# Kernel optimization log

Hardware: AMD Instinct MI355X
Metric: run time of the kernel (lower is better)

Reference implementation:

```python
import jax, jax.numpy as jnp
import numpy as np

EMBED = 256
HEADS = 8
HEAD_DIM = EMBED // HEADS
POOL = 2
H_FEAT = 64
W_FEAT = 64
SCALE = HEAD_DIM ** -0.5
POOL_COMP = float(np.log(POOL * POOL))  # log(pool_size^2) logit compensation


def setup_inputs() -> dict:
    key = jax.random.key(0)
    ks = jax.random.split(key, 11)
    B, Nq = 1, H_FEAT * W_FEAT          # 4096 query tokens (one frame)
    num_spatial = 4 * H_FEAT * W_FEAT   # 4 memory frames -> 16384 spatial tokens
    n_ptr = 64                          # object pointer tokens (not pooled)
    s = 1.0 / np.sqrt(EMBED)
    inp = {
        "q": jax.random.normal(ks[0], (B, Nq, EMBED), jnp.float32),
        "k": jax.random.normal(ks[1], (B, num_spatial + n_ptr, EMBED), jnp.float32),
        "v": jax.random.normal(ks[2], (B, num_spatial + n_ptr, EMBED), jnp.float32),
        "Wq": jax.random.normal(ks[3], (EMBED, EMBED), jnp.float32) * s,
        "bq": jax.random.normal(ks[4], (EMBED,), jnp.float32) * 0.01,
        "Wk": jax.random.normal(ks[5], (EMBED, EMBED), jnp.float32) * s,
        "bk": jax.random.normal(ks[6], (EMBED,), jnp.float32) * 0.01,
        "Wv": jax.random.normal(ks[7], (EMBED, EMBED), jnp.float32) * s,
        "bv": jax.random.normal(ks[8], (EMBED,), jnp.float32) * 0.01,
        "Wo": jax.random.normal(ks[9], (EMBED, EMBED), jnp.float32) * s,
        "bo": jax.random.normal(ks[10], (EMBED,), jnp.float32) * 0.01,
        "num_spatial_mem": num_spatial,
    }
    return inp


def _pool_spatial(tokens, num_spatial):
    """Avg-pool spatial tokens with POOLxPOOL windows; keep pointer tokens."""
    B, N, C = tokens.shape
    sp = tokens[:, :num_spatial, :]
    ptr = tokens[:, num_spatial:, :]
    frames = num_spatial // (H_FEAT * W_FEAT)
    hp, wp = H_FEAT // POOL, W_FEAT // POOL
    sp = sp.reshape(B, frames, hp, POOL, wp, POOL, C).mean(axis=(3, 5))
    sp = sp.reshape(B, frames * hp * wp, C)
    return jnp.concatenate([sp, ptr], axis=1), frames * hp * wp


def _heads(x):
    B, N, _ = x.shape
    return x.reshape(B, N, HEADS, HEAD_DIM).transpose(0, 2, 1, 3)  # (B,h,N,d)


def reference(q, k, v, Wq, bq, Wk, bk, Wv, bv, Wo, bo, num_spatial_mem):
    B, Nq, _ = q.shape
    qp = q @ Wq + bq
    k_pooled, n_sp_pooled = _pool_spatial(k, num_spatial_mem)
    v_pooled, _ = _pool_spatial(v, num_spatial_mem)
    kp = k_pooled @ Wk + bk
    vp = v_pooled @ Wv + bv
    qh, kh, vh = _heads(qp), _heads(kp), _heads(vp)
    logits = jnp.einsum('bhqd,bhkd->bhqk', qh, kh) * SCALE
    # additive bias on the pooled-key subset only
    logits = logits.at[..., :n_sp_pooled].add(POOL_COMP)
    attn = jax.nn.softmax(logits, axis=-1)
    out = jnp.einsum('bhqk,bhkd->bhqd', attn, vh)
    out = out.transpose(0, 2, 1, 3).reshape(B, Nq, EMBED)
    return out @ Wo + bo
```

## Files before the change

kernel.cpp:

```cpp
#include <hip/hip_runtime.h>
#include <hip/hip_bf16.h>
#include <cstdint>

#define NQ 4096
#define NK 4160
#define NSP 16384
#define E 256
#define HD 32
#define SC2E 0.2550348652937f
#define C2_SP  -12.426950408889634f
#define C2_PTR -14.426950408889634f

typedef __attribute__((ext_vector_type(4))) float f32x4;
typedef __attribute__((ext_vector_type(8))) __bf16 bf16x8;
typedef __attribute__((ext_vector_type(4))) __bf16 bf16x4;

__global__ __launch_bounds__(256) void prep_kernel(
    const float* __restrict__ q, const float* __restrict__ k, const float* __restrict__ v,
    const float* __restrict__ Wq, const float* __restrict__ Wk,
    const float* __restrict__ Wv, const float* __restrict__ Wo,
    __bf16* __restrict__ qhi, __bf16* __restrict__ khi, __bf16* __restrict__ vhi,
    __bf16* __restrict__ wthi, __bf16* __restrict__ wtlo)
{
  __shared__ float tl[32][33];
  const int b = blockIdx.x, t = threadIdx.x;
  if (b < 1024) {
    const float4 f = *(const float4*)(q + (size_t)b * 1024 + t * 4);
    bf16x4 o;
    o[0] = (__bf16)f.x; o[1] = (__bf16)f.y; o[2] = (__bf16)f.z; o[3] = (__bf16)f.w;
    *(bf16x4*)(qhi + (size_t)b * 1024 + t * 4) = o;
  } else if (b < 5184) {
    const int p = b - 1024;
    float kv, vv;
    if (p < 4096) {
      int f = p >> 10, hp = (p >> 5) & 31, wp = p & 31;
      size_t r0 = (size_t)(f * 4096 + hp * 128 + wp * 2) * E + t;
      kv = 0.25f * (k[r0] + k[r0 + E] + k[r0 + 64 * E] + k[r0 + 65 * E]);
      vv = 0.25f * (v[r0] + v[r0 + E] + v[r0 + 64 * E] + v[r0 + 65 * E]);
    } else {
      size_t r = (size_t)(NSP + (p - 4096)) * E + t;
      kv = k[r]; vv = v[r];
    }
    khi[(size_t)p * E + t] = (__bf16)kv;
    vhi[(size_t)p * E + t] = (__bf16)vv;
  } else {
    const int wb = b - 5184;
    const int wsel = wb >> 6, tile = wb & 63;
    const float* W = (wsel == 0) ? Wq : (wsel == 1) ? Wk : (wsel == 2) ? Wv : Wo;
    __bf16* oh = wthi + (size_t)wsel * 65536;
    __bf16* ol = wtlo + (size_t)wsel * 65536;
    const int tr = (tile >> 3) * 32, tc = (tile & 7) * 32;
    const int rr = t >> 3, cc = (t & 7) * 4;
    *(float4*)&tl[rr][cc] = *(const float4*)(W + (size_t)(tr + rr) * E + tc + cc);
    __syncthreads();
    bf16x4 hv, lv;
#pragma unroll
    for (int i = 0; i < 4; ++i) {
      float x = tl[cc + i][rr];
      __bf16 bh = (__bf16)x;
      hv[i] = bh;
      lv[i] = (__bf16)(x - (float)bh);
    }
    *(bf16x4*)(oh + (size_t)(tc + rr) * E + tr + cc) = hv;
    *(bf16x4*)(ol + (size_t)(tc + rr) * E + tr + cc) = lv;
  }
}

template<int MODE>
__device__ __forceinline__ void gemm_body(
    const __bf16* __restrict__ X, const __bf16* __restrict__ XL,
    const __bf16* __restrict__ WTH, const __bf16* __restrict__ WTL,
    const float* __restrict__ bias, void* __restrict__ Y, int r0)
{
  const int t = threadIdx.x;
  const int lane = t & 63, ql = lane & 15, g = lane >> 4;
  const int w = t >> 6, c0 = w * 64;

  const __bf16* xp  = X + (size_t)(r0 + ql) * E + g * 8;
  const __bf16* xlp = (MODE == 3) ? XL + (size_t)(r0 + ql) * E + g * 8 : nullptr;
  const __bf16* wh0 = WTH + (size_t)(c0 + ql) * E + g * 8;
  const __bf16* wl0 = (MODE == 3) ? WTL + (size_t)(c0 + ql) * E + g * 8 : nullptr;

  f32x4 acc[4] = {};
#pragma unroll
  for (int k0 = 0; k0 < 8; ++k0) {
    bf16x8 a = *(const bf16x8*)(xp + k0 * 32);
    bf16x8 al{};
    if (MODE == 3) al = *(const bf16x8*)(xlp + k0 * 32);
#pragma unroll
    for (int j = 0; j < 4; ++j) {
      bf16x8 bh = *(const bf16x8*)(wh0 + (size_t)j * 16 * E + k0 * 32);
      if (MODE == 2) {
        acc[j] = __builtin_amdgcn_mfma_f32_16x16x32_bf16(bh, a, acc[j], 0, 0, 0);
      } else {
        acc[j] = __builtin_amdgcn_mfma_f32_16x16x32_bf16(a, bh, acc[j], 0, 0, 0);
        if (MODE == 3) {
          bf16x8 bl = *(const bf16x8*)(wl0 + (size_t)j * 16 * E + k0 * 32);
          acc[j] = __builtin_amdgcn_mfma_f32_16x16x32_bf16(al, bh, acc[j], 0, 0, 0);
          acc[j] = __builtin_amdgcn_mfma_f32_16x16x32_bf16(a, bl, acc[j], 0, 0, 0);
        }
      }
    }
  }

  if (MODE == 0 || MODE == 1) {
    const int NN = (MODE == 0) ? NQ : NK;
#pragma unroll
    for (int j = 0; j < 4; ++j) {
      const int c = c0 + 16 * j + ql;
      const float bv = bias[c];
      const int hh = c >> 5, d = c & 31;
      __bf16* dst = (__bf16*)Y + (size_t)hh * NN * HD + d;
#pragma unroll
      for (int r = 0; r < 4; ++r) {
        const int n = r0 + g * 4 + r;
        float o = acc[j][r] + bv;
        if (MODE == 0) o *= SC2E;
        dst[(size_t)n * HD] = (__bf16)o;
      }
    }
  } else if (MODE == 2) {
    const int n = r0 + ql;
    const int wi = n & 31;
    const int pos = ((wi & 15) >> 2) * 8 + (wi & 3) + 4 * ((wi >> 4) & 1);
    const size_t nb = (size_t)(n >> 5) * 32 + pos;
#pragma unroll
    for (int j = 0; j < 4; ++j)
#pragma unroll
      for (int r = 0; r < 4; ++r) {
        const int ch = c0 + 16 * j + g * 4 + r;
        const int hh = ch >> 5, d = ch & 31;
        ((__bf16*)Y)[(size_t)(hh * HD + d) * NK + nb] = (__bf16)(acc[j][r] + bias[ch]);
      }
  } else {
#pragma unroll
    for (int j = 0; j < 4; ++j) {
      const int c = c0 + 16 * j + ql;
      const float bv = bias[c];
#pragma unroll
      for (int r = 0; r < 4; ++r) {
        const int n = r0 + g * 4 + r;
        ((float*)Y)[(size_t)n * E + c] = acc[j][r] + bv;
      }
    }
  }
}

__global__ __launch_bounds__(256) void gemm_qkv(
    const __bf16* __restrict__ qhi, const __bf16* __restrict__ khi, const __bf16* __restrict__ vhi,
    const __bf16* __restrict__ wthi, const __bf16* __restrict__ wtlo,
    const float* __restrict__ bq, const float* __restrict__ bk, const float* __restrict__ bv,
    __bf16* __restrict__ qb, __bf16* __restrict__ kb, __bf16* __restrict__ vtp)
{
  const int b = blockIdx.x;
  if (b < 256) {
    gemm_body<0>(qhi, nullptr, wthi, nullptr, bq, qb, b * 16);
  } else if (b < 516) {
    gemm_body<1>(khi, nullptr, wthi + 65536, nullptr, bk, kb, (b - 256) * 16);
  } else {
    gemm_body<2>(vhi, nullptr, wthi + 2 * 65536, nullptr, bv, vtp, (b - 516) * 16);
  }
}

__global__ __launch_bounds__(256) void gemm_o(
    const __bf16* __restrict__ ahi, const __bf16* __restrict__ alo,
    const __bf16* __restrict__ wthi, const __bf16* __restrict__ wtlo,
    const float* __restrict__ bo, float* __restrict__ out)
{
  gemm_body<3>(ahi, alo, wthi, wtlo, bo, out, blockIdx.x * 16);
}

__global__ __launch_bounds__(512, 4) void attn_kernel(
    const __bf16* __restrict__ qb, const __bf16* __restrict__ kb,
    const __bf16* __restrict__ vtp, __bf16* __restrict__ ahi, __bf16* __restrict__ alo)
{
  __shared__ float OUT[4][64][36];
  __shared__ float LS[4][64];

  const int t = threadIdx.x;
  const int w = t >> 6, lane = t & 63;
  const int ql = lane & 15, g = lane >> 4;
  const int b = blockIdx.x;
  const int h = b & 7, qt = b >> 3;
  const int n0 = qt * 64;

  bf16x8 bq[4];
#pragma unroll
  for (int f = 0; f < 4; ++f)
    bq[f] = *(const bf16x8*)(qb + ((size_t)h * NQ + n0 + f * 16 + ql) * HD + g * 8);

  const int st = w * 16 + (w < 2 ? w : 2);
  const int nt = 16 + (w < 2 ? 1 : 0);

  const __bf16* kp = kb  + ((size_t)h * NK + st * 32 + ql) * HD + g * 8;
  const __bf16* vp = vtp + ((size_t)(h * HD) + ql) * NK + st * 32 + g * 8;
  const __bf16* vq = vp + (size_t)16 * NK;

  f32x4 o0[4] = {}, o1[4] = {};
  float ls[4] = {0.f, 0.f, 0.f, 0.f};

  bf16x8 kf0 = *(const bf16x8*)(kp);
  bf16x8 kf1 = *(const bf16x8*)(kp + 512);
  bf16x8 vf0 = *(const bf16x8*)(vp);
  bf16x8 vf1 = *(const bf16x8*)(vq);

#define TILE(C2V)                                                                   \
  _Pragma("unroll")                                                                 \
  for (int f = 0; f < 4; ++f) {                                                     \
    f32x4 s0 = __builtin_amdgcn_mfma_f32_16x16x32_bf16(kf0, bq[f], C2V, 0, 0, 0);   \
    f32x4 s1 = __builtin_amdgcn_mfma_f32_16x16x32_bf16(kf1, bq[f], C2V, 0, 0, 0);   \
    float e0 = exp2f(s0[0]), e1 = exp2f(s0[1]), e2 = exp2f(s0[2]), e3 = exp2f(s0[3]);\
    float e4 = exp2f(s1[0]), e5 = exp2f(s1[1]), e6 = exp2f(s1[2]), e7 = exp2f(s1[3]);\
    ls[f] += ((e0 + e1) + (e2 + e3)) + ((e4 + e5) + (e6 + e7));                     \
    bf16x8 p;                                                                       \
    p[0] = (__bf16)e0; p[1] = (__bf16)e1; p[2] = (__bf16)e2; p[3] = (__bf16)e3;     \
    p[4] = (__bf16)e4; p[5] = (__bf16)e5; p[6] = (__bf16)e6; p[7] = (__bf16)e7;     \
    o0[f] = __builtin_amdgcn_mfma_f32_16x16x32_bf16(p, vf0, o0[f], 0, 0, 0);        \
    o1[f] = __builtin_amdgcn_mfma_f32_16x16x32_bf16(p, vf1, o1[f], 0, 0, 0);        \
  }

  for (int it = 0; it < nt - 1; ++it) {
    bf16x8 nk0 = *(const bf16x8*)(kp + (size_t)(it + 1) * 1024);
    bf16x8 nk1 = *(const bf16x8*)(kp + (size_t)(it + 1) * 1024 + 512);
    bf16x8 nv0 = *(const bf16x8*)(vp + (size_t)(it + 1) * 32);
    bf16x8 nv1 = *(const bf16x8*)(vq + (size_t)(it + 1) * 32);
    const float c2 = (st + it < 128) ? C2_SP : C2_PTR;
    const f32x4 c2v = {c2, c2, c2, c2};
    TILE(c2v)
    kf0 = nk0; kf1 = nk1; vf0 = nv0; vf1 = nv1;
  }
  {
    const float c2 = (st + nt - 1 < 128) ? C2_SP : C2_PTR;
    const f32x4 c2v = {c2, c2, c2, c2};
    TILE(c2v)
  }
#undef TILE

#pragma unroll
  for (int f = 0; f < 4; ++f) {
    ls[f] += __shfl_xor(ls[f], 16);
    ls[f] += __shfl_xor(ls[f], 32);
  }

  if (w < 4) {
#pragma unroll
    for (int f = 0; f < 4; ++f) {
#pragma unroll
      for (int r = 0; r < 4; ++r) {
        OUT[w][f * 16 + g * 4 + r][ql]      = o0[f][r];
        OUT[w][f * 16 + g * 4 + r][16 + ql] = o1[f][r];
      }
      if (g == 0) LS[w][f * 16 + ql] = ls[f];
    }
  }
  __syncthreads();
  if (w >= 4) {
    const int w4 = w - 4;
#pragma unroll
    for (int f = 0; f < 4; ++f) {
#pragma unroll
      for (int r = 0; r < 4; ++r) {
        OUT[w4][f * 16 + g * 4 + r][ql]      += o0[f][r];
        OUT[w4][f * 16 + g * 4 + r][16 + ql] += o1[f][r];
      }
      if (g == 0) LS[w4][f * 16 + ql] += ls[f];
    }
  }
  __syncthreads();

  {
    const int q = t >> 3, d0 = (t & 7) * 4;
    f32x4 s = *(const f32x4*)&OUT[0][q][d0];
    float lsum = LS[0][q];
#pragma unroll
    for (int w2 = 1; w2 < 4; ++w2) {
      s += *(const f32x4*)&OUT[w2][q][d0];
      lsum += LS[w2][q];
    }
    const float inv = 1.0f / lsum;
    bf16x4 hv, lv;
#pragma unroll
    for (int i = 0; i < 4; ++i) {
      float o = s[i] * inv;
      __bf16 bh = (__bf16)o;
      hv[i] = bh;
      lv[i] = (__bf16)(o - (float)bh);
    }
    const size_t off = (size_t)(n0 + q) * E + h * HD + d0;
    *(bf16x4*)(ahi + off) = hv;
    *(bf16x4*)(alo + off) = lv;
  }
}

extern "C" void kernel_launch(void* const* d_in, const int* in_sizes, int n_in,
                              void* d_out, int out_size, void* d_ws, size_t ws_size,
                              hipStream_t stream)
{
  const float* q  = (const float*)d_in[0];
  const float* k  = (const float*)d_in[1];
  const float* v  = (const float*)d_in[2];
  const float* Wq = (const float*)d_in[3];
  const float* bq = (const float*)d_in[4];
  const float* Wk = (const float*)d_in[5];
  const float* bk = (const float*)d_in[6];
  const float* Wv = (const float*)d_in[7];
  const float* bv = (const float*)d_in[8];
  const float* Wo = (const float*)d_in[9];
  const float* bo = (const float*)d_in[10];
  float* out = (float*)d_out;

  char* wsp = (char*)d_ws;
  __bf16* qhi  = (__bf16*)(wsp);
  __bf16* khi  = (__bf16*)(wsp + 2097152);
  __bf16* vhi  = (__bf16*)(wsp + 4227072);
  __bf16* wthi = (__bf16*)(wsp + 6356992);
  __bf16* wtlo = (__bf16*)(wsp + 6881280);
  __bf16* qbb  = (__bf16*)(wsp + 7405568);
  __bf16* kbb  = (__bf16*)(wsp + 9502720);
  __bf16* vtp  = (__bf16*)(wsp + 11632640);
  __bf16* ahi  = (__bf16*)(wsp + 13762560);
  __bf16* alo  = (__bf16*)(wsp + 15859712);

  prep_kernel<<<5440, 256, 0, stream>>>(q, k, v, Wq, Wk, Wv, Wo, qhi, khi, vhi, wthi, wtlo);
  gemm_qkv<<<776, 256, 0, stream>>>(qhi, khi, vhi, wthi, wtlo, bq, bk, bv, qbb, kbb, vtp);
  attn_kernel<<<512, 512, 0, stream>>>(qbb, kbb, vtp, ahi, alo);
  gemm_o<<<256, 256, 0, stream>>>(ahi, alo, wthi + 3 * 65536, wtlo + 3 * 65536, bo, out);
}
```

Baseline: 86.01 us.

## Fuse input pooling and bf16 conversion into QKV projection GEMM

After: 69.98 us. -18.6%, faster.

```diff
diff --git a/kernel.cpp b/kernel.cpp
--- a/kernel.cpp
+++ b/kernel.cpp
@@ -15,91 +15,91 @@
 typedef __attribute__((ext_vector_type(8))) __bf16 bf16x8;
 typedef __attribute__((ext_vector_type(4))) __bf16 bf16x4;
 
-__global__ __launch_bounds__(256) void prep_kernel(
-    const float* __restrict__ q, const float* __restrict__ k, const float* __restrict__ v,
+__global__ __launch_bounds__(256) void wprep_kernel(
     const float* __restrict__ Wq, const float* __restrict__ Wk,
     const float* __restrict__ Wv, const float* __restrict__ Wo,
-    __bf16* __restrict__ qhi, __bf16* __restrict__ khi, __bf16* __restrict__ vhi,
     __bf16* __restrict__ wthi, __bf16* __restrict__ wtlo)
 {
   __shared__ float tl[32][33];
   const int b = blockIdx.x, t = threadIdx.x;
-  if (b < 1024) {
-    const float4 f = *(const float4*)(q + (size_t)b * 1024 + t * 4);
-    bf16x4 o;
-    o[0] = (__bf16)f.x; o[1] = (__bf16)f.y; o[2] = (__bf16)f.z; o[3] = (__bf16)f.w;
-    *(bf16x4*)(qhi + (size_t)b * 1024 + t * 4) = o;
-  } else if (b < 5184) {
-    const int p = b - 1024;
-    float kv, vv;
-    if (p < 4096) {
-      int f = p >> 10, hp = (p >> 5) & 31, wp = p & 31;
-      size_t r0 = (size_t)(f * 4096 + hp * 128 + wp * 2) * E + t;
-      kv = 0.25f * (k[r0] + k[r0 + E] + k[r0 + 64 * E] + k[r0 + 65 * E]);
-      vv = 0.25f * (v[r0] + v[r0 + E] + v[r0 + 64 * E] + v[r0 + 65 * E]);
+  const int wsel = b >> 6, tile = b & 63;
+  const float* W = (wsel == 0) ? Wq : (wsel == 1) ? Wk : (wsel == 2) ? Wv : Wo;
+  __bf16* oh = wthi + (size_t)wsel * 65536;
+  __bf16* ol = wtlo + (size_t)wsel * 65536;
+  const int tr = (tile >> 3) * 32, tc = (tile & 7) * 32;
+  const int rr = t >> 3, cc = (t & 7) * 4;
+  *(float4*)&tl[rr][cc] = *(const float4*)(W + (size_t)(tr + rr) * E + tc + cc);
+  __syncthreads();
+  bf16x4 hv, lv;
+#pragma unroll
+  for (int i = 0; i < 4; ++i) {
+    float x = tl[cc + i][rr];
+    __bf16 bh = (__bf16)x;
+    hv[i] = bh;
+    lv[i] = (__bf16)(x - (float)bh);
+  }
+  *(bf16x4*)(oh + (size_t)(tc + rr) * E + tr + cc) = hv;
+  *(bf16x4*)(ol + (size_t)(tc + rr) * E + tr + cc) = lv;
+}
+
+template<int MODE>
+__device__ __forceinline__ void qkv_body(
+    const float* __restrict__ Xsrc, const __bf16* __restrict__ WTH,
+    const float* __restrict__ bias, void* __restrict__ Y, int r0)
+{
+  __shared__ __bf16 Xs[16][264];
+  const int t = threadIdx.x;
+
+  {
+    const int pr = t >> 4, f4 = t & 15;
+    const int p = r0 + pr;
+    float4 x[4];
+    if (MODE == 0) {
+      const float* src = Xsrc + (size_t)p * E + f4 * 4;
+#pragma unroll
+      for (int j = 0; j < 4; ++j) x[j] = *(const float4*)(src + j * 64);
+    } else if (p < 4096) {
+      const int fr = p >> 10, hp = (p >> 5) & 31, wp = p & 31;
+      const float* src = Xsrc + (size_t)(fr * 4096 + hp * 128 + wp * 2) * E + f4 * 4;
+#pragma unroll
+      for (int j = 0; j < 4; ++j) {
+        float4 a = *(const float4*)(src + j * 64);
+        float4 b = *(const float4*)(src + j * 64 + E);
+        float4 c = *(const float4*)(src + j * 64 + 64 * E);
+        float4 d = *(const float4*)(src + j * 64 + 65 * E);
+        x[j].x = 0.25f * (a.x + b.x + c.x + d.x);
+        x[j].y = 0.25f * (a.y + b.y + c.y + d.y);
+        x[j].z = 0.25f * (a.z + b.z + c.z + d.z);
+        x[j].w = 0.25f * (a.w + b.w + c.w + d.w);
+      }
     } else {
-      size_t r = (size_t)(NSP + (p - 4096)) * E + t;
-      kv = k[r]; vv = v[r];
-    }
-    khi[(size_t)p * E + t] = (__bf16)kv;
-    vhi[(size_t)p * E + t] = (__bf16)vv;
-  } else {
-    const int wb = b - 5184;
-    const int wsel = wb >> 6, tile = wb & 63;
-    const float* W = (wsel == 0) ? Wq : (wsel == 1) ? Wk : (wsel == 2) ? Wv : Wo;
-    __bf16* oh = wthi + (size_t)wsel * 65536;
-    __bf16* ol = wtlo + (size_t)wsel * 65536;
-    const int tr = (tile >> 3) * 32, tc = (tile & 7) * 32;
-    const int rr = t >> 3, cc = (t & 7) * 4;
-    *(float4*)&tl[rr][cc] = *(const float4*)(W + (size_t)(tr + rr) * E + tc + cc);
-    __syncthreads();
-    bf16x4 hv, lv;
-#pragma unroll
-    for (int i = 0; i < 4; ++i) {
-      float x = tl[cc + i][rr];
-      __bf16 bh = (__bf16)x;
-      hv[i] = bh;
-      lv[i] = (__bf16)(x - (float)bh);
-    }
-    *(bf16x4*)(oh + (size_t)(tc + rr) * E + tr + cc) = hv;
-    *(bf16x4*)(ol + (size_t)(tc + rr) * E + tr + cc) = lv;
-  }
-}
-
-template<int MODE>
-__device__ __forceinline__ void gemm_body(
-    const __bf16* __restrict__ X, const __bf16* __restrict__ XL,
-    const __bf16* __restrict__ WTH, const __bf16* __restrict__ WTL,
-    const float* __restrict__ bias, void* __restrict__ Y, int r0)
-{
-  const int t = threadIdx.x;
+      const float* src = Xsrc + (size_t)(NSP + p - 4096) * E + f4 * 4;
+#pragma unroll
+      for (int j = 0; j < 4; ++j) x[j] = *(const float4*)(src + j * 64);
+    }
+#pragma unroll
+    for (int j = 0; j < 4; ++j) {
+      bf16x4 o;
+      o[0] = (__bf16)x[j].x; o[1] = (__bf16)x[j].y;
+      o[2] = (__bf16)x[j].z; o[3] = (__bf16)x[j].w;
+      *(bf16x4*)&Xs[pr][f4 * 4 + j * 64] = o;
+    }
+  }
+  __syncthreads();
+
   const int lane = t & 63, ql = lane & 15, g = lane >> 4;
   const int w = t >> 6, c0 = w * 64;
-
-  const __bf16* xp  = X + (size_t)(r0 + ql) * E + g * 8;
-  const __bf16* xlp = (MODE == 3) ? XL + (size_t)(r0 + ql) * E + g * 8 : nullptr;
   const __bf16* wh0 = WTH + (size_t)(c0 + ql) * E + g * 8;
-  const __bf16* wl0 = (MODE == 3) ? WTL + (size_t)(c0 + ql) * E + g * 8 : nullptr;
 
   f32x4 acc[4] = {};
 #pragma unroll
   for (int k0 = 0; k0 < 8; ++k0) {
-    bf16x8 a = *(const bf16x8*)(xp + k0 * 32);
-    bf16x8 al{};
-    if (MODE == 3) al = *(const bf16x8*)(xlp + k0 * 32);
+    bf16x8 a = *(const bf16x8*)&Xs[ql][g * 8 + k0 * 32];
 #pragma unroll
     for (int j = 0; j < 4; ++j) {
       bf16x8 bh = *(const bf16x8*)(wh0 + (size_t)j * 16 * E + k0 * 32);
-      if (MODE == 2) {
-        acc[j] = __builtin_amdgcn_mfma_f32_16x16x32_bf16(bh, a, acc[j], 0, 0, 0);
-      } else {
-        acc[j] = __builtin_amdgcn_mfma_f32_16x16x32_bf16(a, bh, acc[j], 0, 0, 0);
-        if (MODE == 3) {
-          bf16x8 bl = *(const bf16x8*)(wl0 + (size_t)j * 16 * E + k0 * 32);
-          acc[j] = __builtin_amdgcn_mfma_f32_16x16x32_bf16(al, bh, acc[j], 0, 0, 0);
-          acc[j] = __builtin_amdgcn_mfma_f32_16x16x32_bf16(a, bl, acc[j], 0, 0, 0);
-        }
-      }
+      if (MODE == 2) acc[j] = __builtin_amdgcn_mfma_f32_16x16x32_bf16(bh, a, acc[j], 0, 0, 0);
+      else           acc[j] = __builtin_amdgcn_mfma_f32_16x16x32_bf16(a, bh, acc[j], 0, 0, 0);
     }
   }
 
@@ -119,7 +119,7 @@
         dst[(size_t)n * HD] = (__bf16)o;
       }
     }
-  } else if (MODE == 2) {
+  } else {
     const int n = r0 + ql;
     const int wi = n & 31;
     const int pos = ((wi & 15) >> 2) * 8 + (wi & 3) + 4 * ((wi >> 4) & 1);
@@ -132,42 +132,64 @@
         const int hh = ch >> 5, d = ch & 31;
         ((__bf16*)Y)[(size_t)(hh * HD + d) * NK + nb] = (__bf16)(acc[j][r] + bias[ch]);
       }
-  } else {
-#pragma unroll
-    for (int j = 0; j < 4; ++j) {
-      const int c = c0 + 16 * j + ql;
-      const float bv = bias[c];
-#pragma unroll
-      for (int r = 0; r < 4; ++r) {
-        const int n = r0 + g * 4 + r;
-        ((float*)Y)[(size_t)n * E + c] = acc[j][r] + bv;
-      }
-    }
   }
 }
 
 __global__ __launch_bounds__(256) void gemm_qkv(
-    const __bf16* __restrict__ qhi, const __bf16* __restrict__ khi, const __bf16* __restrict__ vhi,
-    const __bf16* __restrict__ wthi, const __bf16* __restrict__ wtlo,
+    const float* __restrict__ q, const float* __restrict__ k, const float* __restrict__ v,
+    const __bf16* __restrict__ wthi,
     const float* __restrict__ bq, const float* __restrict__ bk, const float* __restrict__ bv,
     __bf16* __restrict__ qb, __bf16* __restrict__ kb, __bf16* __restrict__ vtp)
 {
   const int b = blockIdx.x;
   if (b < 256) {
-    gemm_body<0>(qhi, nullptr, wthi, nullptr, bq, qb, b * 16);
+    qkv_body<0>(q, wthi, bq, qb, b * 16);
   } else if (b < 516) {
-    gemm_body<1>(khi, nullptr, wthi + 65536, nullptr, bk, kb, (b - 256) * 16);
+    qkv_body<1>(k, wthi + 65536, bk, kb, (b - 256) * 16);
   } else {
-    gemm_body<2>(vhi, nullptr, wthi + 2 * 65536, nullptr, bv, vtp, (b - 516) * 16);
+    qkv_body<2>(v, wthi + 2 * 65536, bv, vtp, (b - 516) * 16);
   }
 }
 
 __global__ __launch_bounds__(256) void gemm_o(
     const __bf16* __restrict__ ahi, const __bf16* __restrict__ alo,
-    const __bf16* __restrict__ wthi, const __bf16* __restrict__ wtlo,
-    const float* __restrict__ bo, float* __restrict__ out)
-{
-  gemm_body<3>(ahi, alo, wthi, wtlo, bo, out, blockIdx.x * 16);
+    const __bf16* __restrict__ WTH, const __bf16* __restrict__ WTL,
+    const float* __restrict__ bias, float* __restrict__ out)
+{
+  const int r0 = blockIdx.x * 16;
+  const int t = threadIdx.x;
+  const int lane = t & 63, ql = lane & 15, g = lane >> 4;
+  const int w = t >> 6, c0 = w * 64;
+
+  const __bf16* xp  = ahi + (size_t)(r0 + ql) * E + g * 8;
+  const __bf16* xlp = alo + (size_t)(r0 + ql) * E + g * 8;
+  const __bf16* wh0 = WTH + (size_t)(c0 + ql) * E + g * 8;
+  const __bf16* wl0 = WTL + (size_t)(c0 + ql) * E + g * 8;
+
+  f32x4 acc[4] = {};
+#pragma unroll
+  for (int k0 = 0; k0 < 8; ++k0) {
+    bf16x8 a  = *(const bf16x8*)(xp + k0 * 32);
+    bf16x8 al = *(const bf16x8*)(xlp + k0 * 32);
+#pragma unroll
+    for (int j = 0; j < 4; ++j) {
+      bf16x8 bh = *(const bf16x8*)(wh0 + (size_t)j * 16 * E + k0 * 32);
+      bf16x8 bl = *(const bf16x8*)(wl0 + (size_t)j * 16 * E + k0 * 32);
+      acc[j] = __builtin_amdgcn_mfma_f32_16x16x32_bf16(a,  bh, acc[j], 0, 0, 0);
+      acc[j] = __builtin_amdgcn_mfma_f32_16x16x32_bf16(al, bh, acc[j], 0, 0, 0);
+      acc[j] = __builtin_amdgcn_mfma_f32_16x16x32_bf16(a,  bl, acc[j], 0, 0, 0);
+    }
+  }
+#pragma unroll
+  for (int j = 0; j < 4; ++j) {
+    const int c = c0 + 16 * j + ql;
+    const float bv = bias[c];
+#pragma unroll
+    for (int r = 0; r < 4; ++r) {
+      const int n = r0 + g * 4 + r;
+      out[(size_t)n * E + c] = acc[j][r] + bv;
+    }
+  }
 }
 
 __global__ __launch_bounds__(512, 4) void attn_kernel(
@@ -209,8 +231,10 @@
   for (int f = 0; f < 4; ++f) {                                                     \
     f32x4 s0 = __builtin_amdgcn_mfma_f32_16x16x32_bf16(kf0, bq[f], C2V, 0, 0, 0);   \
     f32x4 s1 = __builtin_amdgcn_mfma_f32_16x16x32_bf16(kf1, bq[f], C2V, 0, 0, 0);   \
-    float e0 = exp2f(s0[0]), e1 = exp2f(s0[1]), e2 = exp2f(s0[2]), e3 = exp2f(s0[3]);\
-    float e4 = exp2f(s1[0]), e5 = exp2f(s1[1]), e6 = exp2f(s1[2]), e7 = exp2f(s1[3]);\
+    float e0 = __builtin_amdgcn_exp2f(s0[0]), e1 = __builtin_amdgcn_exp2f(s0[1]);   \
+    float e2 = __builtin_amdgcn_exp2f(s0[2]), e3 = __builtin_amdgcn_exp2f(s0[3]);   \
+    float e4 = __builtin_amdgcn_exp2f(s1[0]), e5 = __builtin_amdgcn_exp2f(s1[1]);   \
+    float e6 = __builtin_amdgcn_exp2f(s1[2]), e7 = __builtin_amdgcn_exp2f(s1[3]);   \
     ls[f] += ((e0 + e1) + (e2 + e3)) + ((e4 + e5) + (e6 + e7));                     \
     bf16x8 p;                                                                       \
     p[0] = (__bf16)e0; p[1] = (__bf16)e1; p[2] = (__bf16)e2; p[3] = (__bf16)e3;     \
@@ -310,19 +334,16 @@
   float* out = (float*)d_out;
 
   char* wsp = (char*)d_ws;
-  __bf16* qhi  = (__bf16*)(wsp);
-  __bf16* khi  = (__bf16*)(wsp + 2097152);
-  __bf16* vhi  = (__bf16*)(wsp + 4227072);
-  __bf16* wthi = (__bf16*)(wsp + 6356992);
-  __bf16* wtlo = (__bf16*)(wsp + 6881280);
-  __bf16* qbb  = (__bf16*)(wsp + 7405568);
-  __bf16* kbb  = (__bf16*)(wsp + 9502720);
-  __bf16* vtp  = (__bf16*)(wsp + 11632640);
-  __bf16* ahi  = (__bf16*)(wsp + 13762560);
-  __bf16* alo  = (__bf16*)(wsp + 15859712);
-
-  prep_kernel<<<5440, 256, 0, stream>>>(q, k, v, Wq, Wk, Wv, Wo, qhi, khi, vhi, wthi, wtlo);
-  gemm_qkv<<<776, 256, 0, stream>>>(qhi, khi, vhi, wthi, wtlo, bq, bk, bv, qbb, kbb, vtp);
+  __bf16* wthi = (__bf16*)(wsp);
+  __bf16* wtlo = (__bf16*)(wsp + 524288);
+  __bf16* qbb  = (__bf16*)(wsp + 1048576);
+  __bf16* kbb  = (__bf16*)(wsp + 3145728);
+  __bf16* vtp  = (__bf16*)(wsp + 5275648);
+  __bf16* ahi  = (__bf16*)(wsp + 7405568);
+  __bf16* alo  = (__bf16*)(wsp + 9502720);
+
+  wprep_kernel<<<256, 256, 0, stream>>>(Wq, Wk, Wv, Wo, wthi, wtlo);
+  gemm_qkv<<<776, 256, 0, stream>>>(q, k, v, wthi, bq, bk, bv, qbb, kbb, vtp);
   attn_kernel<<<512, 512, 0, stream>>>(qbb, kbb, vtp, ahi, alo);
   gemm_o<<<256, 256, 0, stream>>>(ahi, alo, wthi + 3 * 65536, wtlo + 3 * 65536, bo, out);
 }
```
